# Kernel tuning notes

Measured on AMD Instinct MI355X. Metric: run time of the kernel, lower is better.

The kernel has to match this reference:

```python
import jax, jax.numpy as jnp
import numpy as np

N_NODES = 50000
N_EDGES = 800000
IN_F = 96
HID = 64
N_CLS = 32


def setup_inputs() -> dict:
    key = jax.random.key(0)
    k1, k2, k3, k4 = jax.random.split(key, 4)
    x = jax.random.normal(k1, (N_NODES, IN_F), dtype=jnp.float32)
    edge_index = jax.random.randint(k2, (2, N_EDGES), 0, N_NODES, dtype=jnp.int64)
    # xavier_uniform init for weights, zeros for bias
    lim1 = float(np.sqrt(6.0 / (IN_F + HID)))
    lim2 = float(np.sqrt(6.0 / (HID + N_CLS)))
    W1 = jax.random.uniform(k3, (IN_F, HID), minval=-lim1, maxval=lim1, dtype=jnp.float32)
    W2 = jax.random.uniform(k4, (HID, N_CLS), minval=-lim2, maxval=lim2, dtype=jnp.float32)
    b1 = jnp.zeros((HID,), dtype=jnp.float32)
    b2 = jnp.zeros((N_CLS,), dtype=jnp.float32)
    return {"x": x, "edge_index": edge_index, "W1": W1, "b1": b1, "W2": W2, "b2": b2}


def _ghost_conv(h, src, dst, W, b, num_nodes):
    # gather neighbor feats per edge, per-edge matmul, scatter-add, bias
    msg = h[src] @ W                                   # [E, out]
    agg = jax.ops.segment_sum(msg, dst, num_segments=num_nodes)  # [N, out]
    return agg + b


def reference(x, edge_index, W1, b1, W2, b2):
    src, dst = edge_index[0], edge_index[1]
    n = x.shape[0]
    h = jax.nn.relu(_ghost_conv(x, src, dst, W1, b1, n))
    # F.dropout(training=False) is identity in eval mode
    out = _ghost_conv(h, src, dst, W2, b2, n)
    return jax.nn.log_softmax(out, axis=1)
```

## Files before the change

kernel.cpp:

```cpp
#include <hip/hip_runtime.h>
#include <hip/hip_bf16.h>

typedef __attribute__((ext_vector_type(8))) short bf16x8;
typedef __attribute__((ext_vector_type(4))) float f32x4;

#define NBLK 128
#define NBINS_PAD 800
#define BCAP 2048
#define W1LD 104
#define HLD 72

__device__ inline unsigned short f2bf(float f) {
    unsigned u = __float_as_uint(f);
    return (unsigned short)((u + 0x7fffu + ((u >> 16) & 1u)) >> 16);
}
__device__ inline unsigned pack2(float a, float b) {
    return (unsigned)f2bf(a) | ((unsigned)f2bf(b) << 16);
}
__device__ inline float blo(unsigned u) { return __uint_as_float(u << 16); }
__device__ inline float bhi(unsigned u) { return __uint_as_float(u & 0xffff0000u); }

__device__ inline void acc8(float* a, uint4 v) {
    a[0] += blo(v.x); a[1] += bhi(v.x);
    a[2] += blo(v.y); a[3] += bhi(v.y);
    a[4] += blo(v.z); a[5] += bhi(v.z);
    a[6] += blo(v.w); a[7] += bhi(v.w);
}

__global__ __launch_bounds__(256) void fused_hist_gemm1(
        const int* __restrict__ ei, int* __restrict__ counts, int E, int chunk, int nb,
        const float* __restrict__ W1, const float* __restrict__ W2,
        unsigned short* __restrict__ w2t,
        const float* __restrict__ X,
        unsigned short* __restrict__ y1a, unsigned short* __restrict__ y1b, int Mtiles) {
    __shared__ int hist[NBINS_PAD];
    __shared__ unsigned short w1l[64 * W1LD];
    int b = blockIdx.x, t = threadIdx.x;
    if (b < NBLK) {
        for (int i = t; i < NBINS_PAD; i += 256) hist[i] = 0;
        __syncthreads();
        int e0 = b * chunk;
        int n = E - e0; if (n > chunk) n = chunk; if (n < 0) n = 0;
        for (int i = t; i < n; i += 256) atomicAdd(&hist[ei[E + e0 + i] >> 6], 1);
        __syncthreads();
        for (int j = t; j < nb; j += 256) counts[j * NBLK + b] = hist[j];
        return;
    }
    if (b == NBLK) {
        for (int idx = t; idx < 64 * 32; idx += 256) {
            int n = idx / 64, k = idx - n * 64;
            w2t[idx] = f2bf(W2[k * 32 + n]);
        }
        return;
    }
    for (int idx = t; idx < 96 * 64; idx += 256) {
        int n = idx / 96, k = idx - n * 96;
        w1l[n * W1LD + k] = f2bf(W1[k * 64 + n]);
    }
    __syncthreads();
    int wave = (b - NBLK - 1) * 4 + (t >> 6);
    if (wave >= Mtiles) return;
    int lane = t & 63;
    int l15 = lane & 15, quad = lane >> 4;
    const float* arow = X + (long)(wave * 16 + l15) * 96 + quad * 8;
    f32x4 acc[4] = {{0,0,0,0},{0,0,0,0},{0,0,0,0},{0,0,0,0}};
#pragma unroll
    for (int tt = 0; tt < 3; ++tt) {
        float4 p0 = *(const float4*)(arow + tt * 32);
        float4 p1 = *(const float4*)(arow + tt * 32 + 4);
        union { bf16x8 v; unsigned u[4]; } a;
        a.u[0] = pack2(p0.x, p0.y); a.u[1] = pack2(p0.z, p0.w);
        a.u[2] = pack2(p1.x, p1.y); a.u[3] = pack2(p1.z, p1.w);
#pragma unroll
        for (int nt = 0; nt < 4; ++nt) {
            bf16x8 bfr = *(const bf16x8*)(w1l + (nt * 16 + l15) * W1LD + tt * 32 + quad * 8);
            acc[nt] = __builtin_amdgcn_mfma_f32_16x16x32_bf16(a.v, bfr, acc[nt], 0, 0, 0);
        }
    }
    int mbase = wave * 16 + quad * 4;
#pragma unroll
    for (int nt = 0; nt < 4; ++nt) {
        int col = nt * 16 + l15;
        unsigned short* slab = (col < 32) ? y1a : y1b;
        int colh = col & 31;
#pragma unroll
        for (int r = 0; r < 4; ++r)
            slab[(long)(mbase + r) * 32 + colh] = f2bf(acc[nt][r]);
    }
}

__global__ __launch_bounds__(256) void rowscan(int* __restrict__ counts,
                                               int* __restrict__ btot, int nb) {
    int w = (blockIdx.x * 256 + threadIdx.x) >> 6;
    int lane = threadIdx.x & 63;
    if (w >= nb) return;
    int* row = counts + (size_t)w * NBLK;
    int c0 = row[lane * 2], c1 = row[lane * 2 + 1];
    int s = c0 + c1;
#pragma unroll
    for (int o = 1; o < 64; o <<= 1) {
        int tt = __shfl_up(s, o);
        if (lane >= o) s += tt;
    }
    int excl = s - (c0 + c1);
    row[lane * 2] = excl;
    row[lane * 2 + 1] = excl + c0;
    if (lane == 63) btot[w] = s;
}

__global__ __launch_bounds__(256) void blk_place(const int* __restrict__ ei,
                                                 const int* __restrict__ counts,
                                                 unsigned* __restrict__ pairs,
                                                 int E, int chunk, int nb) {
    __shared__ int cur[NBINS_PAD];
    int b = blockIdx.x, t = threadIdx.x;
    for (int j = t; j < nb; j += 256) cur[j] = (j << 11) + counts[j * NBLK + b];
    __syncthreads();
    int e0 = b * chunk;
    int n = E - e0; if (n > chunk) n = chunk; if (n < 0) n = 0;
    for (int i = t; i < n; i += 256) {
        int s = ei[e0 + i], d = ei[E + e0 + i];
        int j = d >> 6;
        int pos = atomicAdd(&cur[j], 1);
        if (pos < ((j + 1) << 11))
            pairs[pos] = (unsigned)s | ((unsigned)(d & 63) << 16);
    }
}

__global__ __launch_bounds__(256) void bucket_fused(
        const unsigned* __restrict__ pairs, const int* __restrict__ btot,
        const uint4* __restrict__ y1a, const uint4* __restrict__ y1b,
        const float* __restrict__ b1, const unsigned short* __restrict__ w2t,
        int2* __restrict__ noderange, int* __restrict__ srcs,
        unsigned short* __restrict__ y2, int N) {
    __shared__ unsigned spk[BCAP];
    __shared__ int lsrc[BCAP];
    __shared__ int cnt64[64], cur64[64], rs[64], re[64];
    __shared__ unsigned short htile[64 * HLD];
    int b = blockIdx.x, t = threadIdx.x;
    int base = b << 11;
    int cnt = btot[b]; if (cnt > BCAP) cnt = BCAP;
    if (t < 64) cnt64[t] = 0;
    __syncthreads();
    for (int i = t; i < cnt; i += 256) {
        unsigned p = pairs[base + i];
        spk[i] = p;
        atomicAdd(&cnt64[(p >> 16) & 63], 1);
    }
    __syncthreads();
    if (t < 64) {
        int v = cnt64[t], x = v;
#pragma unroll
        for (int o = 1; o < 64; o <<= 1) {
            int y = __shfl_up(x, o);
            if (t >= o) x += y;
        }
        int excl = x - v;
        cur64[t] = excl;
        rs[t] = excl;
        re[t] = excl + v;
        int node = b * 64 + t;
        if (node < N) noderange[node] = make_int2(base + excl, base + excl + v);
    }
    __syncthreads();
    for (int i = t; i < cnt; i += 256) {
        unsigned p = spk[i];
        int pos = atomicAdd(&cur64[(p >> 16) & 63], 1);
        lsrc[pos] = (int)(p & 0xffffu);
    }
    __syncthreads();
    for (int i = t; i < cnt; i += 256) srcs[base + i] = lsrc[i];

    int dl = t >> 2, q = t & 3;
    int s0 = rs[dl], s1 = re[dl];
    float a[16];
#pragma unroll
    for (int i = 0; i < 16; ++i) a[i] = 0.f;
    const uint4* yA = y1a + q;
    const uint4* yB = y1b + q;
    int e = s0;
    for (; e + 4 <= s1; e += 4) {
        long r0 = (long)lsrc[e] * 4, r1 = (long)lsrc[e + 1] * 4;
        long r2 = (long)lsrc[e + 2] * 4, r3 = (long)lsrc[e + 3] * 4;
        uint4 a0 = yA[r0], b0 = yB[r0];
        uint4 a1 = yA[r1], b1v = yB[r1];
        uint4 a2 = yA[r2], b2v = yB[r2];
        uint4 a3 = yA[r3], b3v = yB[r3];
        acc8(a, a0); acc8(a + 8, b0);
        acc8(a, a1); acc8(a + 8, b1v);
        acc8(a, a2); acc8(a + 8, b2v);
        acc8(a, a3); acc8(a + 8, b3v);
    }
    for (; e < s1; ++e) {
        long r = (long)lsrc[e] * 4;
        uint4 ua = yA[r], ub = yB[r];
        acc8(a, ua); acc8(a + 8, ub);
    }
    {
        const float* bqA = b1 + q * 8;
        const float* bqB = b1 + 32 + q * 8;
        float v[16];
#pragma unroll
        for (int j = 0; j < 8; ++j) v[j] = fmaxf(a[j] + bqA[j], 0.f);
#pragma unroll
        for (int j = 0; j < 8; ++j) v[8 + j] = fmaxf(a[8 + j] + bqB[j], 0.f);
        uint4 o0, o1;
        o0.x = pack2(v[0], v[1]);   o0.y = pack2(v[2], v[3]);
        o0.z = pack2(v[4], v[5]);   o0.w = pack2(v[6], v[7]);
        o1.x = pack2(v[8], v[9]);   o1.y = pack2(v[10], v[11]);
        o1.z = pack2(v[12], v[13]); o1.w = pack2(v[14], v[15]);
        *(uint4*)(htile + dl * HLD + q * 8) = o0;
        *(uint4*)(htile + dl * HLD + 32 + q * 8) = o1;
    }
    __syncthreads();
    int w = t >> 6, lane = t & 63;
    int l15 = lane & 15, quad = lane >> 4;
    const unsigned short* arow = htile + (w * 16 + l15) * HLD + quad * 8;
    f32x4 acc2[2] = {{0,0,0,0},{0,0,0,0}};
#pragma unroll
    for (int t2 = 0; t2 < 2; ++t2) {
        bf16x8 af = *(const bf16x8*)(arow + t2 * 32);
#pragma unroll
        for (int nt = 0; nt < 2; ++nt) {
            bf16x8 bfr = *(const bf16x8*)(w2t + (long)(nt * 16 + l15) * 64 + t2 * 32 + quad * 8);
            acc2[nt] = __builtin_amdgcn_mfma_f32_16x16x32_bf16(af, bfr, acc2[nt], 0, 0, 0);
        }
    }
    int mbase = b * 64 + w * 16 + quad * 4;
#pragma unroll
    for (int nt = 0; nt < 2; ++nt) {
        int col = nt * 16 + l15;
#pragma unroll
        for (int r = 0; r < 4; ++r) {
            int n = mbase + r;
            if (n < N) y2[(long)n * 32 + col] = f2bf(acc2[nt][r]);
        }
    }
}

__global__ void gather_lsm(const uint4* __restrict__ y2, const int2* __restrict__ rng,
                           const int* __restrict__ srcs, const float* __restrict__ bias,
                           float* __restrict__ out, int N) {
    int gid = blockIdx.x * blockDim.x + threadIdx.x;
    int n = gid >> 2;
    if (n >= N) return;
    int q = gid & 3;
    int2 r01 = rng[n];
    int s0 = r01.x, s1 = r01.y;
    float a[8];
#pragma unroll
    for (int i = 0; i < 8; ++i) a[i] = 0.f;
    const uint4* base = y2 + q;
    int e = s0;
    for (; e + 8 <= s1; e += 8) {
        uint4 u0 = base[(long)srcs[e] * 4],     u1 = base[(long)srcs[e + 1] * 4];
        uint4 u2 = base[(long)srcs[e + 2] * 4], u3 = base[(long)srcs[e + 3] * 4];
        uint4 u4 = base[(long)srcs[e + 4] * 4], u5 = base[(long)srcs[e + 5] * 4];
        uint4 u6 = base[(long)srcs[e + 6] * 4], u7 = base[(long)srcs[e + 7] * 4];
        acc8(a, u0); acc8(a, u1); acc8(a, u2); acc8(a, u3);
        acc8(a, u4); acc8(a, u5); acc8(a, u6); acc8(a, u7);
    }
    for (; e < s1; ++e) acc8(a, base[(long)srcs[e] * 4]);
    const float* bq = bias + q * 8;
    float m = -1e30f;
#pragma unroll
    for (int i = 0; i < 8; ++i) { a[i] += bq[i]; m = fmaxf(m, a[i]); }
    m = fmaxf(m, __shfl_xor(m, 1));
    m = fmaxf(m, __shfl_xor(m, 2));
    float s = 0.f;
#pragma unroll
    for (int i = 0; i < 8; ++i) s += __expf(a[i] - m);
    s += __shfl_xor(s, 1);
    s += __shfl_xor(s, 2);
    float ls = m + __logf(s);
    float* op = out + (long)n * 32 + q * 8;
#pragma unroll
    for (int i = 0; i < 8; ++i) op[i] = a[i] - ls;
}

extern "C" void kernel_launch(void* const* d_in, const int* in_sizes, int n_in,
                              void* d_out, int out_size, void* d_ws, size_t ws_size,
                              hipStream_t stream) {
    const float* x  = (const float*)d_in[0];
    const int*   ei = (const int*)d_in[1];
    const float* W1 = (const float*)d_in[2];
    const float* b1 = (const float*)d_in[3];
    const float* W2 = (const float*)d_in[4];
    const float* b2 = (const float*)d_in[5];
    float* out = (float*)d_out;

    const int N = in_sizes[0] / 96;
    const int E = in_sizes[1] / 2;
    const int nb = (N + 63) / 64;
    const int chunk = (E + NBLK - 1) / NBLK;

    char* p = (char*)d_ws;
    unsigned short* y1a = (unsigned short*)p;     p += (size_t)N * 32 * 2;
    unsigned short* y1b = (unsigned short*)p;     p += (size_t)N * 32 * 2;
    unsigned short* y2  = (unsigned short*)p;     p += (size_t)N * 32 * 2;
    unsigned short* w2t = (unsigned short*)p;     p += 64 * 32 * 2;
    int2* noderange = (int2*)p;                   p += (size_t)N * 8;
    int* counts = (int*)p;                        p += ((size_t)nb * NBLK * 4 + 12) & ~15ull;
    int* btot   = (int*)p;                        p += ((size_t)nb * 4 + 12) & ~15ull;
    unsigned* pairs = (unsigned*)p;               p += (size_t)nb * BCAP * 4;
    int* srcs   = (int*)p;                        p += (size_t)nb * BCAP * 4;

    const int Mtiles = N / 16;
    const int gblocks = (Mtiles + 3) / 4;

    fused_hist_gemm1<<<NBLK + 1 + gblocks, 256, 0, stream>>>(
        ei, counts, E, chunk, nb, W1, W2, w2t, x, y1a, y1b, Mtiles);
    rowscan<<<(nb * 64 + 255) / 256, 256, 0, stream>>>(counts, btot, nb);
    blk_place<<<NBLK, 256, 0, stream>>>(ei, counts, pairs, E, chunk, nb);
    bucket_fused<<<nb, 256, 0, stream>>>(pairs, btot, (const uint4*)y1a, (const uint4*)y1b,
                                         b1, w2t, noderange, srcs, y2, N);
    gather_lsm<<<(N * 4 + 255) / 256, 256, 0, stream>>>(
        (const uint4*)y2, noderange, srcs, b2, out, N);
}
```

Before: 146.8 us.

## Store first-layer projections in FP8 and double histogram block count

The X·W1 projection is now written as one FP8 e4m3 row of 64 bytes instead of two bf16 slabs, which halves the bytes moved by the per-edge gather in the aggregation kernel. The gather loop is unrolled to eight edges and decodes FP8 to float. NBLK also goes from 128 to 256, which spreads the histogram and placement work over more blocks, and rowscan now handles four counts per lane. The cost is a loss of precision in the first-layer messages, which may break tolerance, plus per-element FP8 conversion work.

```diff
diff --git a/kernel.cpp b/kernel.cpp
--- a/kernel.cpp
+++ b/kernel.cpp
@@ -1,10 +1,11 @@
 #include <hip/hip_runtime.h>
 #include <hip/hip_bf16.h>
+#include <hip/hip_fp8.h>
 
 typedef __attribute__((ext_vector_type(8))) short bf16x8;
 typedef __attribute__((ext_vector_type(4))) float f32x4;
 
-#define NBLK 128
+#define NBLK 256
 #define NBINS_PAD 800
 #define BCAP 2048
 #define W1LD 104
@@ -27,12 +28,23 @@
     a[6] += blo(v.w); a[7] += bhi(v.w);
 }
 
+__device__ inline void accf8x4(float* a, unsigned u) {
+    __hip_fp8_e4m3 t;
+    t.__x = (__hip_fp8_storage_t)(u & 0xff);         a[0] += (float)t;
+    t.__x = (__hip_fp8_storage_t)((u >> 8) & 0xff);  a[1] += (float)t;
+    t.__x = (__hip_fp8_storage_t)((u >> 16) & 0xff); a[2] += (float)t;
+    t.__x = (__hip_fp8_storage_t)((u >> 24) & 0xff); a[3] += (float)t;
+}
+__device__ inline void accf8(float* a, uint4 v) {
+    accf8x4(a, v.x); accf8x4(a + 4, v.y); accf8x4(a + 8, v.z); accf8x4(a + 12, v.w);
+}
+
 __global__ __launch_bounds__(256) void fused_hist_gemm1(
         const int* __restrict__ ei, int* __restrict__ counts, int E, int chunk, int nb,
         const float* __restrict__ W1, const float* __restrict__ W2,
         unsigned short* __restrict__ w2t,
         const float* __restrict__ X,
-        unsigned short* __restrict__ y1a, unsigned short* __restrict__ y1b, int Mtiles) {
+        unsigned char* __restrict__ y1f8, int Mtiles) {
     __shared__ int hist[NBINS_PAD];
     __shared__ unsigned short w1l[64 * W1LD];
     int b = blockIdx.x, t = threadIdx.x;
@@ -81,11 +93,11 @@
 #pragma unroll
     for (int nt = 0; nt < 4; ++nt) {
         int col = nt * 16 + l15;
-        unsigned short* slab = (col < 32) ? y1a : y1b;
-        int colh = col & 31;
-#pragma unroll
-        for (int r = 0; r < 4; ++r)
-            slab[(long)(mbase + r) * 32 + colh] = f2bf(acc[nt][r]);
+#pragma unroll
+        for (int r = 0; r < 4; ++r) {
+            __hip_fp8_e4m3 f(acc[nt][r]);
+            y1f8[(long)(mbase + r) * 64 + col] = (unsigned char)f.__x;
+        }
     }
 }
 
@@ -95,16 +107,20 @@
     int lane = threadIdx.x & 63;
     if (w >= nb) return;
     int* row = counts + (size_t)w * NBLK;
-    int c0 = row[lane * 2], c1 = row[lane * 2 + 1];
-    int s = c0 + c1;
+    int c0 = row[lane * 4], c1 = row[lane * 4 + 1];
+    int c2 = row[lane * 4 + 2], c3 = row[lane * 4 + 3];
+    int sum = c0 + c1 + c2 + c3;
+    int s = sum;
 #pragma unroll
     for (int o = 1; o < 64; o <<= 1) {
         int tt = __shfl_up(s, o);
         if (lane >= o) s += tt;
     }
-    int excl = s - (c0 + c1);
-    row[lane * 2] = excl;
-    row[lane * 2 + 1] = excl + c0;
+    int run = s - sum;
+    row[lane * 4] = run;     run += c0;
+    row[lane * 4 + 1] = run; run += c1;
+    row[lane * 4 + 2] = run; run += c2;
+    row[lane * 4 + 3] = run;
     if (lane == 63) btot[w] = s;
 }
 
@@ -129,7 +145,7 @@
 
 __global__ __launch_bounds__(256) void bucket_fused(
         const unsigned* __restrict__ pairs, const int* __restrict__ btot,
-        const uint4* __restrict__ y1a, const uint4* __restrict__ y1b,
+        const uint4* __restrict__ y1f8,
         const float* __restrict__ b1, const unsigned short* __restrict__ w2t,
         int2* __restrict__ noderange, int* __restrict__ srcs,
         unsigned short* __restrict__ y2, int N) {
@@ -176,41 +192,30 @@
     float a[16];
 #pragma unroll
     for (int i = 0; i < 16; ++i) a[i] = 0.f;
-    const uint4* yA = y1a + q;
-    const uint4* yB = y1b + q;
+    const uint4* ybase = y1f8 + q;
     int e = s0;
-    for (; e + 4 <= s1; e += 4) {
-        long r0 = (long)lsrc[e] * 4, r1 = (long)lsrc[e + 1] * 4;
-        long r2 = (long)lsrc[e + 2] * 4, r3 = (long)lsrc[e + 3] * 4;
-        uint4 a0 = yA[r0], b0 = yB[r0];
-        uint4 a1 = yA[r1], b1v = yB[r1];
-        uint4 a2 = yA[r2], b2v = yB[r2];
-        uint4 a3 = yA[r3], b3v = yB[r3];
-        acc8(a, a0); acc8(a + 8, b0);
-        acc8(a, a1); acc8(a + 8, b1v);
-        acc8(a, a2); acc8(a + 8, b2v);
-        acc8(a, a3); acc8(a + 8, b3v);
-    }
-    for (; e < s1; ++e) {
-        long r = (long)lsrc[e] * 4;
-        uint4 ua = yA[r], ub = yB[r];
-        acc8(a, ua); acc8(a + 8, ub);
-    }
+    for (; e + 8 <= s1; e += 8) {
+        uint4 u0 = ybase[(long)lsrc[e] * 4],     u1 = ybase[(long)lsrc[e + 1] * 4];
+        uint4 u2 = ybase[(long)lsrc[e + 2] * 4], u3 = ybase[(long)lsrc[e + 3] * 4];
+        uint4 u4 = ybase[(long)lsrc[e + 4] * 4], u5 = ybase[(long)lsrc[e + 5] * 4];
+        uint4 u6 = ybase[(long)lsrc[e + 6] * 4], u7 = ybase[(long)lsrc[e + 7] * 4];
+        accf8(a, u0); accf8(a, u1); accf8(a, u2); accf8(a, u3);
+        accf8(a, u4); accf8(a, u5); accf8(a, u6); accf8(a, u7);
+    }
+    for (; e < s1; ++e) accf8(a, ybase[(long)lsrc[e] * 4]);
     {
-        const float* bqA = b1 + q * 8;
-        const float* bqB = b1 + 32 + q * 8;
+        const float* bq = b1 + q * 16;
         float v[16];
 #pragma unroll
-        for (int j = 0; j < 8; ++j) v[j] = fmaxf(a[j] + bqA[j], 0.f);
-#pragma unroll
-        for (int j = 0; j < 8; ++j) v[8 + j] = fmaxf(a[8 + j] + bqB[j], 0.f);
+        for (int j = 0; j < 16; ++j) v[j] = fmaxf(a[j] + bq[j], 0.f);
         uint4 o0, o1;
         o0.x = pack2(v[0], v[1]);   o0.y = pack2(v[2], v[3]);
         o0.z = pack2(v[4], v[5]);   o0.w = pack2(v[6], v[7]);
         o1.x = pack2(v[8], v[9]);   o1.y = pack2(v[10], v[11]);
         o1.z = pack2(v[12], v[13]); o1.w = pack2(v[14], v[15]);
-        *(uint4*)(htile + dl * HLD + q * 8) = o0;
-        *(uint4*)(htile + dl * HLD + 32 + q * 8) = o1;
+        uint4* hp = (uint4*)(htile + dl * HLD + q * 16);
+        hp[0] = o0;
+        hp[1] = o1;
     }
     __syncthreads();
     int w = t >> 6, lane = t & 63;
@@ -295,10 +300,9 @@
     const int chunk = (E + NBLK - 1) / NBLK;
 
     char* p = (char*)d_ws;
-    unsigned short* y1a = (unsigned short*)p;     p += (size_t)N * 32 * 2;
-    unsigned short* y1b = (unsigned short*)p;     p += (size_t)N * 32 * 2;
-    unsigned short* y2  = (unsigned short*)p;     p += (size_t)N * 32 * 2;
-    unsigned short* w2t = (unsigned short*)p;     p += 64 * 32 * 2;
+    unsigned char*  y1f8 = (unsigned char*)p;     p += (size_t)N * 64;
+    unsigned short* y2   = (unsigned short*)p;    p += (size_t)N * 32 * 2;
+    unsigned short* w2t  = (unsigned short*)p;    p += 64 * 32 * 2;
     int2* noderange = (int2*)p;                   p += (size_t)N * 8;
     int* counts = (int*)p;                        p += ((size_t)nb * NBLK * 4 + 12) & ~15ull;
     int* btot   = (int*)p;                        p += ((size_t)nb * 4 + 12) & ~15ull;
@@ -309,10 +313,10 @@
     const int gblocks = (Mtiles + 3) / 4;
 
     fused_hist_gemm1<<<NBLK + 1 + gblocks, 256, 0, stream>>>(
-        ei, counts, E, chunk, nb, W1, W2, w2t, x, y1a, y1b, Mtiles);
+        ei, counts, E, chunk, nb, W1, W2, w2t, x, y1f8, Mtiles);
     rowscan<<<(nb * 64 + 255) / 256, 256, 0, stream>>>(counts, btot, nb);
     blk_place<<<NBLK, 256, 0, stream>>>(ei, counts, pairs, E, chunk, nb);
-    bucket_fused<<<nb, 256, 0, stream>>>(pairs, btot, (const uint4*)y1a, (const uint4*)y1b,
+    bucket_fused<<<nb, 256, 0, stream>>>(pairs, btot, (const uint4*)y1f8,
                                          b1, w2t, noderange, srcs, y2, N);
     gather_lsm<<<(N * 4 + 255) / 256, 256, 0, stream>>>(
         (const uint4*)y2, noderange, srcs, b2, out, N);
```

New measurement: 142.1 us (median of 2 runs). 3.2% less time.
